# Performance work log

Measured on AMD Instinct MI355X. Metric: run time of the kernel, lower is better.

The kernel has to match this reference:

```python
import jax, jax.numpy as jnp
import numpy as np

N = 8192        # number of nodes
IN_CH = 256     # in_channels
OUT_CH = 256    # out_channels


def setup_inputs() -> dict:
    key = jax.random.key(0)
    k1, k2, k3, k4 = jax.random.split(key, 4)
    A = jax.random.normal(k1, (N, N), dtype=jnp.float32)
    # degree-like matrix: only its diagonal matters; keep it strictly positive
    D = jax.random.uniform(k2, (N, N), dtype=jnp.float32, minval=0.5, maxval=2.0)
    H = jax.random.normal(k3, (N, IN_CH), dtype=jnp.float32)
    W = jax.random.normal(k4, (IN_CH, OUT_CH), dtype=jnp.float32)  # nn.Parameter, normal_() init
    return {"A": A, "D": D, "H": H, "W": W}


def reference(A, D, H, W):
    # Original: D_ = diag(diag(rsqrt(D))); T = D_ @ A @ D_ @ H @ W
    # diag-matrix matmuls are mathematically row/column scalings; same math, no O(n^3) diag mm.
    d = jax.lax.rsqrt(jnp.diagonal(D))          # [N], rsqrt of diagonal entries
    A_norm = A * d[:, None] * d[None, :]        # D^-1/2 A D^-1/2, fused elementwise
    return (A_norm @ H) @ W                     # [N, OUT_CH]
```

## Files before the change

### kernel.cpp

```cpp
#include <hip/hip_runtime.h>
#include <hip/hip_bf16.h>

#define NN 8192
#define CH 256

typedef float f32x4 __attribute__((ext_vector_type(4)));
typedef __bf16 bf16x8 __attribute__((ext_vector_type(8)));

union FragU { uint4 u; bf16x8 h; };

static __device__ __forceinline__ unsigned short f2bf(float f) {
  union { float f; unsigned int u; } v; v.f = f;
  unsigned int x = v.u;
  return (unsigned short)((x + 0x7fffu + ((x >> 16) & 1u)) >> 16);
}

__global__ __launch_bounds__(256) void k_prep(const float* __restrict__ Hm,
                                              const float* __restrict__ Dm,
                                              const float* __restrict__ Wm,
                                              unsigned short* __restrict__ HT,
                                              unsigned short* __restrict__ WT) {
  __shared__ float tile[64][65];
  int bx = blockIdx.x, t = threadIdx.x;
  bool isH = bx < 512;
  int b = isH ? bx : bx - 512;
  int r0 = (b >> 2) * 64;
  int j0 = (b & 3) * 64;
  const float* src = isH ? Hm : Wm;

  int r = t >> 2;
  int cq = (t & 3) * 16;
  float dval = isH ? rsqrtf(Dm[(size_t)(r0 + r) * (NN + 1)]) : 1.0f;
  const float* p = src + (size_t)(r0 + r) * CH + j0 + cq;
#pragma unroll
  for (int u = 0; u < 4; ++u) {
    float4 v = *(const float4*)(p + u * 4);
    tile[r][cq + u * 4 + 0] = v.x * dval;
    tile[r][cq + u * 4 + 1] = v.y * dval;
    tile[r][cq + u * 4 + 2] = v.z * dval;
    tile[r][cq + u * 4 + 3] = v.w * dval;
  }
  __syncthreads();
  int j = t >> 2;
  int kq = (t & 3) * 16;
  __align__(16) unsigned short ov[16];
#pragma unroll
  for (int i = 0; i < 16; ++i) ov[i] = f2bf(tile[kq + i][j]);
  unsigned short* dst = isH ? (HT + (size_t)(j0 + j) * NN + r0 + kq)
                            : (WT + (size_t)(j0 + j) * CH + r0 + kq);
  *(uint4*)dst = *(uint4*)ov;
  *(uint4*)(dst + 8) = *(uint4*)(ov + 8);
}

__global__ __launch_bounds__(256) void k_gemm1(const float* __restrict__ A,
                                               const unsigned short* __restrict__ HT,
                                               float* __restrict__ P) {
  __shared__ unsigned short As[64][72];
  __shared__ unsigned short Bs[256][72];
  int bx = blockIdx.x;
  int strip = bx >> 1, s = bx & 1;
  int i0 = strip * 64;
  int kbase = s * 4096;
  int t = threadIdx.x, l = t & 63, w = t >> 6;
  int lan = l & 15, quad = l >> 4;

  int ar = t >> 2, aq = (t & 3) * 16;
  const float* Ap = A + (size_t)(i0 + ar) * NN + kbase + aq;
  int bn = t >> 3, bc = (t & 7) * 8;
  const unsigned short* Bp = HT + (size_t)bn * NN + kbase + bc;

  float4 areg[4];
  uint4 breg[8];
  f32x4 acc[4][4];
#pragma unroll
  for (int mt = 0; mt < 4; ++mt)
#pragma unroll
    for (int nt = 0; nt < 4; ++nt)
#pragma unroll
      for (int c = 0; c < 4; ++c) acc[mt][nt][c] = 0.0f;

#pragma unroll
  for (int u = 0; u < 4; ++u) areg[u] = *(const float4*)(Ap + u * 4);
#pragma unroll
  for (int j = 0; j < 8; ++j) breg[j] = *(const uint4*)(Bp + (size_t)j * 32 * NN);

  for (int kt = 0; kt < 64; ++kt) {
    __syncthreads();
#pragma unroll
    for (int u = 0; u < 4; ++u) {
      float4 v = areg[u];
      union { unsigned short h[4]; uint2 u2; } pk;
      pk.h[0] = f2bf(v.x); pk.h[1] = f2bf(v.y); pk.h[2] = f2bf(v.z); pk.h[3] = f2bf(v.w);
      *(uint2*)&As[ar][aq + u * 4] = pk.u2;
    }
#pragma unroll
    for (int j = 0; j < 8; ++j) *(uint4*)&Bs[j * 32 + bn][bc] = breg[j];
    __syncthreads();
    if (kt < 63) {
      const float* Ap2 = Ap + (kt + 1) * 64;
#pragma unroll
      for (int u = 0; u < 4; ++u) areg[u] = *(const float4*)(Ap2 + u * 4);
      const unsigned short* Bp2 = Bp + (kt + 1) * 64;
#pragma unroll
      for (int j = 0; j < 8; ++j) breg[j] = *(const uint4*)(Bp2 + (size_t)j * 32 * NN);
    }
#pragma unroll
    for (int ss = 0; ss < 2; ++ss) {
      FragU af[4], bfr[4];
#pragma unroll
      for (int mt = 0; mt < 4; ++mt)
        af[mt].u = *(const uint4*)&As[mt * 16 + lan][ss * 32 + quad * 8];
#pragma unroll
      for (int nt = 0; nt < 4; ++nt)
        bfr[nt].u = *(const uint4*)&Bs[w * 64 + nt * 16 + lan][ss * 32 + quad * 8];
#pragma unroll
      for (int mt = 0; mt < 4; ++mt)
#pragma unroll
        for (int nt = 0; nt < 4; ++nt)
          acc[mt][nt] = __builtin_amdgcn_mfma_f32_16x16x32_bf16(af[mt].h, bfr[nt].h, acc[mt][nt], 0, 0, 0);
    }
  }
  float* Pp = P + (size_t)s * NN * CH;
#pragma unroll
  for (int mt = 0; mt < 4; ++mt) {
    int i = i0 + mt * 16 + quad * 4;
#pragma unroll
    for (int nt = 0; nt < 4; ++nt) {
      int jc = w * 64 + nt * 16 + lan;
#pragma unroll
      for (int r = 0; r < 4; ++r)
        Pp[(size_t)(i + r) * CH + jc] = acc[mt][nt][r];
    }
  }
}

__global__ __launch_bounds__(256) void k_gemm2(const float* __restrict__ P,
                                               const float* __restrict__ Dm,
                                               const unsigned short* __restrict__ WT,
                                               float* __restrict__ out) {
  __shared__ unsigned short Gs[32][264];
  __shared__ unsigned short Ws[64][264];
  int bx = blockIdx.x, t = threadIdx.x, l = t & 63, w = t >> 6;
  int lan = l & 15, quad = l >> 4;
  int i0 = bx * 32;
  {
    int r = t >> 3, c0 = (t & 7) * 32;
    float dval = rsqrtf(Dm[(size_t)(i0 + r) * (NN + 1)]);
    const float* p0 = P + (size_t)(i0 + r) * CH + c0;
    const float* p1 = p0 + (size_t)NN * CH;
    __align__(16) unsigned short g[32];
#pragma unroll
    for (int u = 0; u < 8; ++u) {
      float4 a = *(const float4*)(p0 + u * 4);
      float4 b = *(const float4*)(p1 + u * 4);
      g[u * 4 + 0] = f2bf((a.x + b.x) * dval);
      g[u * 4 + 1] = f2bf((a.y + b.y) * dval);
      g[u * 4 + 2] = f2bf((a.z + b.z) * dval);
      g[u * 4 + 3] = f2bf((a.w + b.w) * dval);
    }
#pragma unroll
    for (int u = 0; u < 4; ++u) *(uint4*)&Gs[r][c0 + u * 8] = *(uint4*)(g + u * 8);
  }
  for (int jt = 0; jt < 4; ++jt) {
    __syncthreads();
    {
      int nrow = t >> 2, cb = (t & 3) * 64;
      const unsigned short* wp = WT + (size_t)(jt * 64 + nrow) * CH + cb;
#pragma unroll
      for (int u = 0; u < 8; ++u) *(uint4*)&Ws[nrow][cb + u * 8] = *(const uint4*)(wp + u * 8);
    }
    __syncthreads();
    f32x4 acc[2];
#pragma unroll
    for (int mt = 0; mt < 2; ++mt)
#pragma unroll
      for (int c = 0; c < 4; ++c) acc[mt][c] = 0.0f;
#pragma unroll
    for (int ks = 0; ks < 8; ++ks) {
      FragU af0, af1, bfr;
      af0.u = *(const uint4*)&Gs[lan][ks * 32 + quad * 8];
      af1.u = *(const uint4*)&Gs[16 + lan][ks * 32 + quad * 8];
      bfr.u = *(const uint4*)&Ws[w * 16 + lan][ks * 32 + quad * 8];
      acc[0] = __builtin_amdgcn_mfma_f32_16x16x32_bf16(af0.h, bfr.h, acc[0], 0, 0, 0);
      acc[1] = __builtin_amdgcn_mfma_f32_16x16x32_bf16(af1.h, bfr.h, acc[1], 0, 0, 0);
    }
#pragma unroll
    for (int mt = 0; mt < 2; ++mt) {
      int i = i0 + mt * 16 + quad * 4;
      int jc = jt * 64 + w * 16 + lan;
#pragma unroll
      for (int r = 0; r < 4; ++r)
        out[(size_t)(i + r) * CH + jc] = acc[mt][r];
    }
  }
}

extern "C" void kernel_launch(void* const* d_in, const int* in_sizes, int n_in,
                              void* d_out, int out_size, void* d_ws, size_t ws_size,
                              hipStream_t stream) {
  const float* A  = (const float*)d_in[0];
  const float* Dm = (const float*)d_in[1];
  const float* Hm = (const float*)d_in[2];
  const float* Wm = (const float*)d_in[3];
  float* out = (float*)d_out;
  char* ws = (char*)d_ws;
  unsigned short* HT = (unsigned short*)ws;
  unsigned short* WT = (unsigned short*)(ws + (size_t)4194304);
  float* P = (float*)(ws + (size_t)4194304 + 131072);

  hipLaunchKernelGGL(k_prep,  dim3(528), dim3(256), 0, stream, Hm, Dm, Wm, HT, WT);
  hipLaunchKernelGGL(k_gemm1, dim3(256), dim3(256), 0, stream, A, HT, P);
  hipLaunchKernelGGL(k_gemm2, dim3(256), dim3(256), 0, stream, P, Dm, WT, out);
}
```

Measured before the change: 621.3 us.

## Load H fragments directly to registers, deepen split-K, simplify second GEMM

The first GEMM no longer stages H through shared memory. Each wave loads its B fragments straight from global memory into registers and double-buffers both A and B across two k-steps. Split-K rises from 2 to 4 when the workspace allows, giving 512 blocks, and launch bounds request 2 blocks per CU. The second GEMM now uses 16-row blocks, sums SK partial slices and reads W fragments directly from global memory. This removes LDS traffic and barriers for B and raises parallelism, at the cost of more partial-sum traffic and more register pressure.

```diff
diff --git a/kernel.cpp b/kernel.cpp
--- a/kernel.cpp
+++ b/kernel.cpp
@@ -52,25 +52,25 @@
   *(uint4*)(dst + 8) = *(uint4*)(ov + 8);
 }
 
-__global__ __launch_bounds__(256) void k_gemm1(const float* __restrict__ A,
-                                               const unsigned short* __restrict__ HT,
-                                               float* __restrict__ P) {
+template <int SK>
+__global__ __launch_bounds__(256, 2) void k_gemm1(const float* __restrict__ A,
+                                                  const unsigned short* __restrict__ HT,
+                                                  float* __restrict__ P) {
+  constexpr int KC = NN / SK;
+  constexpr int NIT = KC / 64;
   __shared__ unsigned short As[64][72];
-  __shared__ unsigned short Bs[256][72];
-  int bx = blockIdx.x;
-  int strip = bx >> 1, s = bx & 1;
-  int i0 = strip * 64;
-  int kbase = s * 4096;
-  int t = threadIdx.x, l = t & 63, w = t >> 6;
-  int lan = l & 15, quad = l >> 4;
-
-  int ar = t >> 2, aq = (t & 3) * 16;
+  const int bx = blockIdx.x;
+  const int strip = bx / SK, s = bx % SK;
+  const int i0 = strip * 64, kbase = s * KC;
+  const int t = threadIdx.x, l = t & 63, w = t >> 6;
+  const int lan = l & 15, quad = l >> 4;
+
+  const int ar = t >> 2, aq = (t & 3) * 16;
   const float* Ap = A + (size_t)(i0 + ar) * NN + kbase + aq;
-  int bn = t >> 3, bc = (t & 7) * 8;
-  const unsigned short* Bp = HT + (size_t)bn * NN + kbase + bc;
-
-  float4 areg[4];
-  uint4 breg[8];
+  const unsigned short* Bb = HT + (size_t)(w * 64 + lan) * NN + kbase + quad * 8;
+
+  float4 a0[4], a1[4];
+  FragU bc[8], bn[8];
   f32x4 acc[4][4];
 #pragma unroll
   for (int mt = 0; mt < 4; ++mt)
@@ -79,120 +79,126 @@
 #pragma unroll
       for (int c = 0; c < 4; ++c) acc[mt][nt][c] = 0.0f;
 
-#pragma unroll
-  for (int u = 0; u < 4; ++u) areg[u] = *(const float4*)(Ap + u * 4);
-#pragma unroll
-  for (int j = 0; j < 8; ++j) breg[j] = *(const uint4*)(Bp + (size_t)j * 32 * NN);
-
-  for (int kt = 0; kt < 64; ++kt) {
-    __syncthreads();
+  auto loadA = [&](float4 (&dst)[4], int kt) {
+    const float* p = Ap + kt * 64;
+#pragma unroll
+    for (int u = 0; u < 4; ++u) dst[u] = *(const float4*)(p + u * 4);
+  };
+  auto loadB = [&](FragU (&dst)[8], int kt) {
+    const unsigned short* p = Bb + kt * 64;
+#pragma unroll
+    for (int ss = 0; ss < 2; ++ss)
+#pragma unroll
+      for (int nt = 0; nt < 4; ++nt)
+        dst[ss * 4 + nt].u = *(const uint4*)(p + (size_t)nt * 16 * NN + ss * 32);
+  };
+  auto storeA = [&](float4 (&src)[4]) {
 #pragma unroll
     for (int u = 0; u < 4; ++u) {
-      float4 v = areg[u];
+      float4 v = src[u];
       union { unsigned short h[4]; uint2 u2; } pk;
       pk.h[0] = f2bf(v.x); pk.h[1] = f2bf(v.y); pk.h[2] = f2bf(v.z); pk.h[3] = f2bf(v.w);
       *(uint2*)&As[ar][aq + u * 4] = pk.u2;
     }
-#pragma unroll
-    for (int j = 0; j < 8; ++j) *(uint4*)&Bs[j * 32 + bn][bc] = breg[j];
-    __syncthreads();
-    if (kt < 63) {
-      const float* Ap2 = Ap + (kt + 1) * 64;
-#pragma unroll
-      for (int u = 0; u < 4; ++u) areg[u] = *(const float4*)(Ap2 + u * 4);
-      const unsigned short* Bp2 = Bp + (kt + 1) * 64;
-#pragma unroll
-      for (int j = 0; j < 8; ++j) breg[j] = *(const uint4*)(Bp2 + (size_t)j * 32 * NN);
-    }
+  };
+  auto compute = [&](FragU (&b)[8]) {
 #pragma unroll
     for (int ss = 0; ss < 2; ++ss) {
-      FragU af[4], bfr[4];
+      FragU af[4];
 #pragma unroll
       for (int mt = 0; mt < 4; ++mt)
         af[mt].u = *(const uint4*)&As[mt * 16 + lan][ss * 32 + quad * 8];
 #pragma unroll
-      for (int nt = 0; nt < 4; ++nt)
-        bfr[nt].u = *(const uint4*)&Bs[w * 64 + nt * 16 + lan][ss * 32 + quad * 8];
-#pragma unroll
       for (int mt = 0; mt < 4; ++mt)
 #pragma unroll
         for (int nt = 0; nt < 4; ++nt)
-          acc[mt][nt] = __builtin_amdgcn_mfma_f32_16x16x32_bf16(af[mt].h, bfr[nt].h, acc[mt][nt], 0, 0, 0);
-    }
-  }
-  float* Pp = P + (size_t)s * NN * CH;
-#pragma unroll
-  for (int mt = 0; mt < 4; ++mt) {
-    int i = i0 + mt * 16 + quad * 4;
-#pragma unroll
-    for (int nt = 0; nt < 4; ++nt) {
-      int jc = w * 64 + nt * 16 + lan;
+          acc[mt][nt] = __builtin_amdgcn_mfma_f32_16x16x32_bf16(af[mt].h, b[ss * 4 + nt].h,
+                                                                acc[mt][nt], 0, 0, 0);
+    }
+  };
+
+  loadA(a0, 0);
+  loadA(a1, 1);
+  loadB(bc, 0);
+
+  for (int kt = 0; kt < NIT; kt += 2) {
+    __syncthreads();
+    storeA(a0);
+    __syncthreads();
+    if (kt + 2 < NIT) loadA(a0, kt + 2);
+    loadB(bn, kt + 1);
+    compute(bc);
+    __syncthreads();
+    storeA(a1);
+    __syncthreads();
+    if (kt + 3 < NIT) loadA(a1, kt + 3);
+    if (kt + 2 < NIT) loadB(bc, kt + 2);
+    compute(bn);
+  }
+
+  float* Pp = P + ((size_t)s * NN + i0) * CH;
+#pragma unroll
+  for (int mt = 0; mt < 4; ++mt)
+#pragma unroll
+    for (int nt = 0; nt < 4; ++nt)
 #pragma unroll
       for (int r = 0; r < 4; ++r)
-        Pp[(size_t)(i + r) * CH + jc] = acc[mt][nt][r];
-    }
-  }
-}
-
+        Pp[(size_t)(mt * 16 + quad * 4 + r) * CH + w * 64 + nt * 16 + lan] = acc[mt][nt][r];
+}
+
+template <int SK>
 __global__ __launch_bounds__(256) void k_gemm2(const float* __restrict__ P,
                                                const float* __restrict__ Dm,
                                                const unsigned short* __restrict__ WT,
                                                float* __restrict__ out) {
-  __shared__ unsigned short Gs[32][264];
-  __shared__ unsigned short Ws[64][264];
-  int bx = blockIdx.x, t = threadIdx.x, l = t & 63, w = t >> 6;
-  int lan = l & 15, quad = l >> 4;
-  int i0 = bx * 32;
+  __shared__ unsigned short Gs[16][264];
+  const int bx = blockIdx.x, t = threadIdx.x, l = t & 63, w = t >> 6;
+  const int lan = l & 15, quad = l >> 4;
+  const int i0 = bx * 16;
   {
-    int r = t >> 3, c0 = (t & 7) * 32;
+    const int r = t >> 4, c0 = (t & 15) * 16;
     float dval = rsqrtf(Dm[(size_t)(i0 + r) * (NN + 1)]);
-    const float* p0 = P + (size_t)(i0 + r) * CH + c0;
-    const float* p1 = p0 + (size_t)NN * CH;
-    __align__(16) unsigned short g[32];
-#pragma unroll
-    for (int u = 0; u < 8; ++u) {
-      float4 a = *(const float4*)(p0 + u * 4);
-      float4 b = *(const float4*)(p1 + u * 4);
-      g[u * 4 + 0] = f2bf((a.x + b.x) * dval);
-      g[u * 4 + 1] = f2bf((a.y + b.y) * dval);
-      g[u * 4 + 2] = f2bf((a.z + b.z) * dval);
-      g[u * 4 + 3] = f2bf((a.w + b.w) * dval);
-    }
-#pragma unroll
-    for (int u = 0; u < 4; ++u) *(uint4*)&Gs[r][c0 + u * 8] = *(uint4*)(g + u * 8);
-  }
-  for (int jt = 0; jt < 4; ++jt) {
-    __syncthreads();
-    {
-      int nrow = t >> 2, cb = (t & 3) * 64;
-      const unsigned short* wp = WT + (size_t)(jt * 64 + nrow) * CH + cb;
-#pragma unroll
-      for (int u = 0; u < 8; ++u) *(uint4*)&Ws[nrow][cb + u * 8] = *(const uint4*)(wp + u * 8);
-    }
-    __syncthreads();
-    f32x4 acc[2];
-#pragma unroll
-    for (int mt = 0; mt < 2; ++mt)
-#pragma unroll
-      for (int c = 0; c < 4; ++c) acc[mt][c] = 0.0f;
-#pragma unroll
-    for (int ks = 0; ks < 8; ++ks) {
-      FragU af0, af1, bfr;
-      af0.u = *(const uint4*)&Gs[lan][ks * 32 + quad * 8];
-      af1.u = *(const uint4*)&Gs[16 + lan][ks * 32 + quad * 8];
-      bfr.u = *(const uint4*)&Ws[w * 16 + lan][ks * 32 + quad * 8];
-      acc[0] = __builtin_amdgcn_mfma_f32_16x16x32_bf16(af0.h, bfr.h, acc[0], 0, 0, 0);
-      acc[1] = __builtin_amdgcn_mfma_f32_16x16x32_bf16(af1.h, bfr.h, acc[1], 0, 0, 0);
-    }
-#pragma unroll
-    for (int mt = 0; mt < 2; ++mt) {
-      int i = i0 + mt * 16 + quad * 4;
-      int jc = jt * 64 + w * 16 + lan;
-#pragma unroll
-      for (int r = 0; r < 4; ++r)
-        out[(size_t)(i + r) * CH + jc] = acc[mt][r];
-    }
-  }
+    const float* pp = P + (size_t)(i0 + r) * CH + c0;
+    __align__(16) unsigned short g[16];
+#pragma unroll
+    for (int u = 0; u < 4; ++u) {
+      float sx = 0.f, sy = 0.f, sz = 0.f, sw = 0.f;
+#pragma unroll
+      for (int s = 0; s < SK; ++s) {
+        float4 v = *(const float4*)(pp + (size_t)s * NN * CH + u * 4);
+        sx += v.x; sy += v.y; sz += v.z; sw += v.w;
+      }
+      g[u * 4 + 0] = f2bf(sx * dval);
+      g[u * 4 + 1] = f2bf(sy * dval);
+      g[u * 4 + 2] = f2bf(sz * dval);
+      g[u * 4 + 3] = f2bf(sw * dval);
+    }
+    *(uint4*)&Gs[r][c0] = *(uint4*)g;
+    *(uint4*)&Gs[r][c0 + 8] = *(uint4*)(g + 8);
+  }
+  __syncthreads();
+  const int j0 = w * 64;
+  f32x4 acc[4];
+#pragma unroll
+  for (int nt = 0; nt < 4; ++nt)
+#pragma unroll
+    for (int c = 0; c < 4; ++c) acc[nt][c] = 0.0f;
+#pragma unroll
+  for (int ks = 0; ks < 8; ++ks) {
+    FragU af;
+    af.u = *(const uint4*)&Gs[lan][ks * 32 + quad * 8];
+#pragma unroll
+    for (int nt = 0; nt < 4; ++nt) {
+      FragU bw;
+      bw.u = *(const uint4*)&WT[(size_t)(j0 + nt * 16 + lan) * CH + ks * 32 + quad * 8];
+      acc[nt] = __builtin_amdgcn_mfma_f32_16x16x32_bf16(af.h, bw.h, acc[nt], 0, 0, 0);
+    }
+  }
+#pragma unroll
+  for (int nt = 0; nt < 4; ++nt)
+#pragma unroll
+    for (int r = 0; r < 4; ++r)
+      out[(size_t)(i0 + quad * 4 + r) * CH + j0 + nt * 16 + lan] = acc[nt][r];
 }
 
 extern "C" void kernel_launch(void* const* d_in, const int* in_sizes, int n_in,
@@ -208,7 +214,15 @@
   unsigned short* WT = (unsigned short*)(ws + (size_t)4194304);
   float* P = (float*)(ws + (size_t)4194304 + 131072);
 
-  hipLaunchKernelGGL(k_prep,  dim3(528), dim3(256), 0, stream, Hm, Dm, Wm, HT, WT);
-  hipLaunchKernelGGL(k_gemm1, dim3(256), dim3(256), 0, stream, A, HT, P);
-  hipLaunchKernelGGL(k_gemm2, dim3(256), dim3(256), 0, stream, P, Dm, WT, out);
-}
+  const size_t base = 4194304 + 131072;
+  const size_t needS4 = base + (size_t)4 * NN * CH * 4;
+
+  hipLaunchKernelGGL(k_prep, dim3(528), dim3(256), 0, stream, Hm, Dm, Wm, HT, WT);
+  if (ws_size >= needS4) {
+    hipLaunchKernelGGL((k_gemm1<4>), dim3(512), dim3(256), 0, stream, A, HT, P);
+    hipLaunchKernelGGL((k_gemm2<4>), dim3(512), dim3(256), 0, stream, P, Dm, WT, out);
+  } else {
+    hipLaunchKernelGGL((k_gemm1<2>), dim3(256), dim3(256), 0, stream, A, HT, P);
+    hipLaunchKernelGGL((k_gemm2<2>), dim3(512), dim3(256), 0, stream, P, Dm, WT, out);
+  }
+}
```

Result: faster. 507.7 us (-18.3%).
